# Kernel optimization log

Measured on AMD Instinct MI355X. Metric: run time of the kernel, lower is better.

The kernel has to match this reference:

```python
import jax, jax.numpy as jnp
import numpy as np

B, SQ, SK, D, H = 4, 2048, 2048, 1024, 16
HD = D // H
LN_EPS = 1e-5


def setup_inputs() -> dict:
    key = jax.random.key(0)
    ks = jax.random.split(key, 16)
    s = 0.02
    return {
        "query": jax.random.normal(ks[0], (B, SQ, D), jnp.float32),
        "key": jax.random.normal(ks[1], (B, SK, D), jnp.float32),
        "value": jax.random.normal(ks[2], (B, SK, D), jnp.float32),
        "attention_mask": jax.random.randint(ks[3], (B, 1, 1, SK), 0, 2, jnp.int32),
        "relative_position_bias": jax.random.normal(ks[4], (1, H, SQ, SK), jnp.float32) * s,
        "Wq": jax.random.normal(ks[5], (D, D), jnp.float32) * s,
        "bq": jnp.zeros((D,), jnp.float32),
        "Wk": jax.random.normal(ks[6], (D, D), jnp.float32) * s,
        "bk": jnp.zeros((D,), jnp.float32),
        "Wv": jax.random.normal(ks[7], (D, D), jnp.float32) * s,
        "bv": jnp.zeros((D,), jnp.float32),
        "Wo": jax.random.normal(ks[8], (D, D), jnp.float32) * s,
        "bo": jnp.zeros((D,), jnp.float32),
        "ln_gamma": jnp.ones((D,), jnp.float32),
        "ln_beta": jnp.zeros((D,), jnp.float32),
    }


def reference(query, key, value, attention_mask, relative_position_bias,
              Wq, bq, Wk, bk, Wv, bv, Wo, bo, ln_gamma, ln_beta):
    # projections (torch Linear: x @ W.T + b)
    q = query @ Wq.T + bq   # [B,Sq,D]
    k = key @ Wk.T + bk     # [B,Sk,D]
    v = value @ Wv.T + bv   # [B,Sk,D]
    # split heads -> [B,H,S,hd]
    q = q.reshape(B, SQ, H, HD).transpose(0, 2, 1, 3)
    k = k.reshape(B, SK, H, HD).transpose(0, 2, 1, 3)
    v = v.reshape(B, SK, H, HD).transpose(0, 2, 1, 3)
    scores = jnp.einsum('bhqd,bhkd->bhqk', q, k) / jnp.sqrt(jnp.float32(HD))
    scores = scores + relative_position_bias
    scores = jnp.where(attention_mask == 0, -jnp.inf, scores)
    weights = jax.nn.softmax(scores, axis=-1)  # [B,H,Sq,Sk]
    ctx = jnp.einsum('bhqk,bhkd->bhqd', weights, v)
    ctx = ctx.transpose(0, 2, 1, 3).reshape(B, SQ, D)
    out = ctx @ Wo.T + bo
    x = query + out
    mu = jnp.mean(x, axis=-1, keepdims=True)
    var = jnp.var(x, axis=-1, keepdims=True)
    return (x - mu) * jax.lax.rsqrt(var + LN_EPS) * ln_gamma + ln_beta
```

## Files before the change

kernel.cpp:

```cpp
#include <hip/hip_runtime.h>
#include <hip/hip_bf16.h>

#define B_   4
#define SQ_  2048
#define SK_  2048
#define D_   1024
#define H_   16
#define HD_  64

#define LOG2E 1.4426950408889634f

typedef __bf16 bf16_t;
typedef bf16_t bf16x8 __attribute__((ext_vector_type(8)));
typedef bf16_t bf16x4 __attribute__((ext_vector_type(4)));
typedef float  f32x4  __attribute__((ext_vector_type(4)));
typedef int    i32x4  __attribute__((ext_vector_type(4)));
typedef unsigned u32x2 __attribute__((ext_vector_type(2)));



__device__ __forceinline__ void gll16(const bf16_t* g, bf16_t* l) {
    __builtin_amdgcn_global_load_lds(
        (const __attribute__((address_space(1))) unsigned int*)g,
        (__attribute__((address_space(3))) unsigned int*)l, 16, 0, 0);
}
__device__ __forceinline__ void gll16f(const float* g, float* l) {
    __builtin_amdgcn_global_load_lds(
        (const __attribute__((address_space(1))) unsigned int*)g,
        (__attribute__((address_space(3))) unsigned int*)l, 16, 0, 0);
}

__global__ __launch_bounds__(256) void cvt_bf16(
    const float* __restrict__ p0, const float* __restrict__ p1,
    const float* __restrict__ p2, const float* __restrict__ p3,
    bf16_t* __restrict__ d, int n)
{
    int y = blockIdx.y;
    const float* s = (y == 0) ? p0 : (y == 1) ? p1 : (y == 2) ? p2 : p3;
    int i = (blockIdx.x * 256 + threadIdx.x) * 8;
    f32x4 a = *(const f32x4*)(s + i);
    f32x4 b = *(const f32x4*)(s + i + 4);
    bf16x8 o;
    #pragma unroll
    for (int j = 0; j < 4; j++) { o[j] = (bf16_t)a[j]; o[4 + j] = (bf16_t)b[j]; }
    *(bf16x8*)(d + (size_t)y * n + i) = o;
}

__global__ __launch_bounds__(256) void gemm_qkv(
    const float* __restrict__ xq, const float* __restrict__ xk, const float* __restrict__ xv,
    const bf16_t* __restrict__ wb,
    const float* __restrict__ bq, const float* __restrict__ bk, const float* __restrict__ bv,
    bf16_t* __restrict__ oq, bf16_t* __restrict__ ok, bf16_t* __restrict__ ov)
{
    __shared__ __align__(16) float  lAf[2][4096];
    __shared__ __align__(16) bf16_t lB[2][4096];

    int z = blockIdx.z;
    const float* A = (z == 0) ? xq : (z == 1) ? xk : xv;
    const bf16_t* Bm = wb + (size_t)z * 1024 * 1024;
    const float* bias = (z == 0) ? bq : (z == 1) ? bk : bv;
    bf16_t* out = (z == 0) ? oq : (z == 1) ? ok : ov;

    int tid = threadIdx.x;
    int w = tid >> 6, l = tid & 63, lr = l & 15, lg = l >> 4;
    int m0 = blockIdx.x * 128, n0 = blockIdx.y * 128;
    int wm = (w >> 1) * 64, wn = (w & 1) * 64;

    f32x4 zero4 = {0.f, 0.f, 0.f, 0.f};
    f32x4 acc[4][4];
    #pragma unroll
    for (int i = 0; i < 4; i++)
        #pragma unroll
        for (int j = 0; j < 4; j++) acc[i][j] = zero4;

    int as0 = tid, as1 = tid + 256, as2 = tid + 512, as3 = tid + 768;
    int ar0 = as0 >> 3, ar1 = as1 >> 3, ar2 = as2 >> 3, ar3 = as3 >> 3;
    const float* a_p0 = A + (size_t)(m0 + ar0) * 1024 + (((as0 & 7) ^ (ar0 & 7)) * 4);
    const float* a_p1 = A + (size_t)(m0 + ar1) * 1024 + (((as1 & 7) ^ (ar1 & 7)) * 4);
    const float* a_p2 = A + (size_t)(m0 + ar2) * 1024 + (((as2 & 7) ^ (ar2 & 7)) * 4);
    const float* a_p3 = A + (size_t)(m0 + ar3) * 1024 + (((as3 & 7) ^ (ar3 & 7)) * 4);

    int bs0 = tid, bs1 = tid + 256;
    int br0 = bs0 >> 2, br1 = bs1 >> 2;
    const bf16_t* b_p0 = Bm + (size_t)(n0 + br0) * 1024 + (((bs0 & 3) ^ ((br0 >> 1) & 3)) * 8);
    const bf16_t* b_p1 = Bm + (size_t)(n0 + br1) * 1024 + (((bs1 & 3) ^ ((br1 >> 1) & 3)) * 8);

    auto stage = [&](int buf, int kt) {
        gll16f(a_p0 + kt * 32, &lAf[buf][as0 * 4]);
        gll16f(a_p1 + kt * 32, &lAf[buf][as1 * 4]);
        gll16f(a_p2 + kt * 32, &lAf[buf][as2 * 4]);
        gll16f(a_p3 + kt * 32, &lAf[buf][as3 * 4]);
        gll16(b_p0 + kt * 32, &lB[buf][bs0 * 8]);
        gll16(b_p1 + kt * 32, &lB[buf][bs1 * 8]);
    };

    stage(0, 0);
    int buf = 0;
    #pragma unroll 1
    for (int kt = 0; kt < 32; ++kt) {
        __syncthreads();
        if (kt + 1 < 32) stage(buf ^ 1, kt + 1);
        bf16x8 af[4], bfr[4];
        #pragma unroll
        for (int i = 0; i < 4; i++) {
            int ra = wm + i * 16 + lr;
            int e = ra & 7;
            const float* arow = &lAf[buf][ra * 32];
            f32x4 lo = *(const f32x4*)(arow + ((( lg * 2)      ^ e) * 4));
            f32x4 hi = *(const f32x4*)(arow + ((((lg * 2) + 1) ^ e) * 4));
            bf16x8 a8;
            #pragma unroll
            for (int j = 0; j < 4; j++) { a8[j] = (bf16_t)lo[j]; a8[4 + j] = (bf16_t)hi[j]; }
            af[i] = a8;
            int rb = wn + i * 16 + lr;
            bfr[i] = *(const bf16x8*)&lB[buf][rb * 32 + ((lg ^ ((rb >> 1) & 3)) * 8)];
        }
        #pragma unroll
        for (int mi = 0; mi < 4; mi++)
            #pragma unroll
            for (int ni = 0; ni < 4; ni++)
                acc[mi][ni] = __builtin_amdgcn_mfma_f32_16x16x32_bf16(af[mi], bfr[ni], acc[mi][ni], 0, 0, 0);
        buf ^= 1;
    }

    #pragma unroll
    for (int mi = 0; mi < 4; mi++) {
        int row = m0 + wm + mi * 16 + lg * 4;
        int bb_ = row >> 11;
        int s   = row & 2047;
        #pragma unroll
        for (int ni = 0; ni < 4; ni++) {
            int col = n0 + wn + ni * 16 + lr;
            int hh = col >> 6, d6 = col & 63;
            float bval = bias[col];
            if (z == 0) {
                size_t obase = (((size_t)bb_ * H_ + hh) * SQ_ + s) * HD_ + d6;
                #pragma unroll
                for (int r = 0; r < 4; r++)
                    out[obase + (size_t)r * HD_] =
                        (bf16_t)((acc[mi][ni][r] + bval) * (0.125f * LOG2E));
            } else if (z == 1) {
                int kt = s >> 6, kpb = s & 63;
                size_t tb = (((size_t)bb_ * H_ + hh) * 32 + kt) * 4096;
                #pragma unroll
                for (int r = 0; r < 4; r++) {
                    int kp = kpb + r;
                    out[tb + (size_t)kp * 64 + (((d6 >> 3) ^ (kp & 7)) * 8) + (d6 & 7)] =
                        (bf16_t)(acc[mi][ni][r] + bval);
                }
            } else {
                int kt = s >> 6, kpb = s & 63;
                int chunk = ((kpb >> 5) & 1) * 4 + ((kpb >> 2) & 3);
                int jb    = ((kpb >> 4) & 1) * 4;
                size_t tb = (((size_t)bb_ * H_ + hh) * 32 + kt) * 4096;
                bf16x4 o4;
                #pragma unroll
                for (int r = 0; r < 4; r++) o4[r] = (bf16_t)(acc[mi][ni][r] + bval);
                *(bf16x4*)(out + tb + (size_t)d6 * 64 + ((chunk ^ (d6 & 7)) * 8) + jb) = o4;
            }
        }
    }
}

__global__ __launch_bounds__(256) void gemm_out(
    const bf16_t* __restrict__ A, const bf16_t* __restrict__ Bm,
    const float* __restrict__ bias, const float* __restrict__ resid,
    bf16_t* __restrict__ out)
{
    __shared__ __align__(16) bf16_t lA[2][4096];
    __shared__ __align__(16) bf16_t lB[2][4096];

    int tid = threadIdx.x;
    int w = tid >> 6, l = tid & 63, lr = l & 15, lg = l >> 4;
    int m0 = blockIdx.x * 128, n0 = blockIdx.y * 128;
    int wm = (w >> 1) * 64, wn = (w & 1) * 64;

    f32x4 zero4 = {0.f, 0.f, 0.f, 0.f};
    f32x4 acc[4][4];
    #pragma unroll
    for (int i = 0; i < 4; i++)
        #pragma unroll
        for (int j = 0; j < 4; j++) acc[i][j] = zero4;

    int s0 = tid, s1 = 256 + tid;
    int r0 = s0 >> 2, c0 = s0 & 3, r1 = s1 >> 2, c1 = s1 & 3;
    const bf16_t* a0 = A + (size_t)(m0 + r0) * 1024 + ((c0 ^ ((r0 >> 1) & 3)) * 8);
    const bf16_t* a1 = A + (size_t)(m0 + r1) * 1024 + ((c1 ^ ((r1 >> 1) & 3)) * 8);
    const bf16_t* b0 = Bm + (size_t)(n0 + r0) * 1024 + ((c0 ^ ((r0 >> 1) & 3)) * 8);
    const bf16_t* b1 = Bm + (size_t)(n0 + r1) * 1024 + ((c1 ^ ((r1 >> 1) & 3)) * 8);

    auto stage = [&](int buf, int kt) {
        gll16(a0 + kt * 32, &lA[buf][s0 * 8]);
        gll16(a1 + kt * 32, &lA[buf][s1 * 8]);
        gll16(b0 + kt * 32, &lB[buf][s0 * 8]);
        gll16(b1 + kt * 32, &lB[buf][s1 * 8]);
    };

    stage(0, 0);
    int buf = 0;
    #pragma unroll 1
    for (int kt = 0; kt < 32; ++kt) {
        __syncthreads();
        if (kt + 1 < 32) stage(buf ^ 1, kt + 1);
        bf16x8 af[4], bfr[4];
        #pragma unroll
        for (int i = 0; i < 4; i++) {
            int ra = wm + i * 16 + lr;
            af[i] = *(const bf16x8*)&lA[buf][ra * 32 + ((lg ^ ((ra >> 1) & 3)) * 8)];
            int rb = wn + i * 16 + lr;
            bfr[i] = *(const bf16x8*)&lB[buf][rb * 32 + ((lg ^ ((rb >> 1) & 3)) * 8)];
        }
        #pragma unroll
        for (int mi = 0; mi < 4; mi++)
            #pragma unroll
            for (int ni = 0; ni < 4; ni++)
                acc[mi][ni] = __builtin_amdgcn_mfma_f32_16x16x32_bf16(af[mi], bfr[ni], acc[mi][ni], 0, 0, 0);
        buf ^= 1;
    }

    #pragma unroll
    for (int mi = 0; mi < 4; mi++) {
        int row = m0 + wm + mi * 16 + lg * 4;
        #pragma unroll
        for (int ni = 0; ni < 4; ni++) {
            int col = n0 + wn + ni * 16 + lr;
            float bval = bias[col];
            #pragma unroll
            for (int r = 0; r < 4; r++) {
                size_t o = (size_t)(row + r) * D_ + col;
                out[o] = (bf16_t)(acc[mi][ni][r] + bval + resid[o]);
            }
        }
    }
}

__global__ __launch_bounds__(256) void attn_kernel(
    const bf16_t* __restrict__ qg, const bf16_t* __restrict__ kgt,
    const bf16_t* __restrict__ vgt, const float* __restrict__ bias,
    const int* __restrict__ mask, bf16_t* __restrict__ ctx)
{
    __shared__ __align__(16) bf16_t ksh[2][8192];
    __shared__ __align__(16) bf16_t vsh[2][8192];
    __shared__ __align__(8) unsigned char mlds[256];

    int x = blockIdx.x;
    int g8 = x & 7;
    int rest = x >> 3;
    int b  = rest & 3;
    int tt = ((rest >> 2) << 3) | g8;
    int h  = tt >> 4;
    int qt = tt & 15;

    int tid = threadIdx.x;
    int w   = tid >> 6;
    int l   = tid & 63;
    int q16 = l & 15;
    int g   = l >> 4;
    int g4  = g * 4;

    int qrow0 = qt * 128 + w * 16 + q16;
    int qrow1 = qrow0 + 64;
    const bf16_t* qbase = qg + ((size_t)b * H_ + h) * SQ_ * HD_;
    bf16x8 qf00 = *(const bf16x8*)(qbase + (size_t)qrow0 * HD_ + g * 8);
    bf16x8 qf01 = *(const bf16x8*)(qbase + (size_t)qrow0 * HD_ + 32 + g * 8);
    bf16x8 qf10 = *(const bf16x8*)(qbase + (size_t)qrow1 * HD_ + g * 8);
    bf16x8 qf11 = *(const bf16x8*)(qbase + (size_t)qrow1 * HD_ + 32 + g * 8);

    const bf16_t* kt_base = kgt + ((size_t)b * H_ + h) * 32 * 4096;
    const bf16_t* vt_base = vgt + ((size_t)b * H_ + h) * 32 * 4096;
    const float* bias_row0 = bias + ((size_t)h * SQ_ + qrow0) * SK_;
    const float* bias_row1 = bias + ((size_t)h * SQ_ + qrow1) * SK_;

    f32x4 zero4 = {0.f, 0.f, 0.f, 0.f};
    f32x4 oacc0[4], oacc1[4];
    #pragma unroll
    for (int i = 0; i < 4; i++) { oacc0[i] = zero4; oacc1[i] = zero4; }
    f32x4 lacc0 = zero4, lacc1 = zero4;

    bf16x8 ones;
    #pragma unroll
    for (int i = 0; i < 8; i++) ones[i] = (bf16_t)1.0f;

    auto stagePair = [&](int buf, int pt) {
        const bf16_t* ks = kt_base + (size_t)pt * 8192 + tid * 8;
        const bf16_t* vs = vt_base + (size_t)pt * 8192 + tid * 8;
        #pragma unroll
        for (int c = 0; c < 4; c++) {
            gll16(ks + c * 2048, &ksh[buf][c * 2048 + tid * 8]);
            gll16(vs + c * 2048, &vsh[buf][c * 2048 + tid * 8]);
        }
    };

    auto body = [&](const bf16_t* kb, const bf16_t* vb, int t) {
        f32x4 bb0[4], bb1[4];
        const float* bp0 = bias_row0 + t * 64 + g4;
        const float* bp1 = bias_row1 + t * 64 + g4;
        #pragma unroll
        for (int ni = 0; ni < 4; ni++) {
            bb0[ni] = *(const f32x4*)(bp0 + ni * 16);
            bb1[ni] = *(const f32x4*)(bp1 + ni * 16);
        }
        u32x2 mm = *(const u32x2*)&mlds[t * 8];
        unsigned lo = mm[0], hi = mm[1];

        f32x4 s0[4], s1[4];
        __builtin_amdgcn_s_setprio(1);
        #pragma unroll
        for (int ni = 0; ni < 4; ni++) {
            int krow = ni * 16 + q16;
            const bf16_t* kr = kb + krow * 64;
            bf16x8 kf0 = *(const bf16x8*)(kr + ((g       ^ (krow & 7)) * 8));
            bf16x8 kf1 = *(const bf16x8*)(kr + (((4 + g) ^ (krow & 7)) * 8));
            s0[ni] = zero4; s1[ni] = zero4;
            s0[ni] = __builtin_amdgcn_mfma_f32_16x16x32_bf16(kf0, qf00, s0[ni], 0, 0, 0);
            s0[ni] = __builtin_amdgcn_mfma_f32_16x16x32_bf16(kf1, qf01, s0[ni], 0, 0, 0);
            s1[ni] = __builtin_amdgcn_mfma_f32_16x16x32_bf16(kf0, qf10, s1[ni], 0, 0, 0);
            s1[ni] = __builtin_amdgcn_mfma_f32_16x16x32_bf16(kf1, qf11, s1[ni], 0, 0, 0);
        }
        __builtin_amdgcn_s_setprio(0);

        unsigned n0_ = (lo >> g4) & 0xF;
        unsigned n1_ = (lo >> (16 + g4)) & 0xF;
        unsigned n2_ = (hi >> g4) & 0xF;
        unsigned n3_ = (hi >> (16 + g4)) & 0xF;

        bf16x8 pA0, pA1, pB0, pB1;
        #pragma unroll
        for (int r = 0; r < 4; r++) {
            float b00 = ((n0_ >> r) & 1) ? bb0[0][r] : -30000.f;
            float b01 = ((n1_ >> r) & 1) ? bb0[1][r] : -30000.f;
            float b02 = ((n2_ >> r) & 1) ? bb0[2][r] : -30000.f;
            float b03 = ((n3_ >> r) & 1) ? bb0[3][r] : -30000.f;
            pA0[r]     = (bf16_t)__builtin_amdgcn_exp2f(fmaf(b00, LOG2E, s0[0][r]));
            pA0[4 + r] = (bf16_t)__builtin_amdgcn_exp2f(fmaf(b01, LOG2E, s0[1][r]));
            pA1[r]     = (bf16_t)__builtin_amdgcn_exp2f(fmaf(b02, LOG2E, s0[2][r]));
            pA1[4 + r] = (bf16_t)__builtin_amdgcn_exp2f(fmaf(b03, LOG2E, s0[3][r]));
            float b10 = ((n0_ >> r) & 1) ? bb1[0][r] : -30000.f;
            float b11 = ((n1_ >> r) & 1) ? bb1[1][r] : -30000.f;
            float b12 = ((n2_ >> r) & 1) ? bb1[2][r] : -30000.f;
            float b13 = ((n3_ >> r) & 1) ? bb1[3][r] : -30000.f;
            pB0[r]     = (bf16_t)__builtin_amdgcn_exp2f(fmaf(b10, LOG2E, s1[0][r]));
            pB0[4 + r] = (bf16_t)__builtin_amdgcn_exp2f(fmaf(b11, LOG2E, s1[1][r]));
            pB1[r]     = (bf16_t)__builtin_amdgcn_exp2f(fmaf(b12, LOG2E, s1[2][r]));
            pB1[4 + r] = (bf16_t)__builtin_amdgcn_exp2f(fmaf(b13, LOG2E, s1[3][r]));
        }

        __builtin_amdgcn_s_setprio(1);
        lacc0 = __builtin_amdgcn_mfma_f32_16x16x32_bf16(ones, pA0, lacc0, 0, 0, 0);
        lacc0 = __builtin_amdgcn_mfma_f32_16x16x32_bf16(ones, pA1, lacc0, 0, 0, 0);
        lacc1 = __builtin_amdgcn_mfma_f32_16x16x32_bf16(ones, pB0, lacc1, 0, 0, 0);
        lacc1 = __builtin_amdgcn_mfma_f32_16x16x32_bf16(ones, pB1, lacc1, 0, 0, 0);
        #pragma unroll
        for (int nd = 0; nd < 4; nd++) {
            int vrow = nd * 16 + q16;
            const bf16_t* vr = vb + vrow * 64;
            bf16x8 vf0 = *(const bf16x8*)(vr + ((g       ^ (vrow & 7)) * 8));
            bf16x8 vf1 = *(const bf16x8*)(vr + (((4 + g) ^ (vrow & 7)) * 8));
            oacc0[nd] = __builtin_amdgcn_mfma_f32_16x16x32_bf16(vf0, pA0, oacc0[nd], 0, 0, 0);
            oacc0[nd] = __builtin_amdgcn_mfma_f32_16x16x32_bf16(vf1, pA1, oacc0[nd], 0, 0, 0);
            oacc1[nd] = __builtin_amdgcn_mfma_f32_16x16x32_bf16(vf0, pB0, oacc1[nd], 0, 0, 0);
            oacc1[nd] = __builtin_amdgcn_mfma_f32_16x16x32_bf16(vf1, pB1, oacc1[nd], 0, 0, 0);
        }
        __builtin_amdgcn_s_setprio(0);
    };

    stagePair(0, 0);
    {
        const int* mp = mask + (size_t)b * SK_ + tid * 8;
        i32x4 u0 = *(const i32x4*)mp;
        i32x4 u1 = *(const i32x4*)(mp + 4);
        unsigned by = 0;
        #pragma unroll
        for (int j = 0; j < 4; j++) by |= (u0[j] != 0 ? 1u : 0u) << j;
        #pragma unroll
        for (int j = 0; j < 4; j++) by |= (u1[j] != 0 ? 1u : 0u) << (4 + j);
        mlds[tid] = (unsigned char)by;
    }
    __syncthreads();

    #pragma unroll 1
    for (int pt = 0; pt < 16; ++pt) {
        int buf = pt & 1;
        if (pt + 1 < 16) stagePair(buf ^ 1, pt + 1);
        body(&ksh[buf][0],    &vsh[buf][0],    2 * pt);
        body(&ksh[buf][4096], &vsh[buf][4096], 2 * pt + 1);
        __syncthreads();
    }

    float l_r0 = lacc0[0];
    float l_r1 = lacc1[0];
    float inv0 = (l_r0 > 0.f) ? 1.0f / l_r0 : 0.f;
    float inv1 = (l_r1 > 0.f) ? 1.0f / l_r1 : 0.f;

    bf16_t* cp0 = ctx + ((size_t)b * SQ_ + qrow0) * D_ + (size_t)h * HD_;
    bf16_t* cp1 = ctx + ((size_t)b * SQ_ + qrow1) * D_ + (size_t)h * HD_;
    #pragma unroll
    for (int nd = 0; nd < 4; nd++) {
        bf16x4 o4, o5;
        #pragma unroll
        for (int r = 0; r < 4; r++) {
            o4[r] = (bf16_t)(oacc0[nd][r] * inv0);
            o5[r] = (bf16_t)(oacc1[nd][r] * inv1);
        }
        *(bf16x4*)(cp0 + nd * 16 + g4) = o4;
        *(bf16x4*)(cp1 + nd * 16 + g4) = o5;
    }
}

__global__ __launch_bounds__(256) void ln_kernel(
    const bf16_t* __restrict__ x, const float* __restrict__ gamma,
    const float* __restrict__ beta, float* __restrict__ out)
{
    int row = blockIdx.x;
    int t = threadIdx.x;
    const bf16_t* src = x + (size_t)row * D_;
    bf16x4 v4 = *(const bf16x4*)(src + t * 4);
    f32x4 v;
    #pragma unroll
    for (int i = 0; i < 4; i++) v[i] = (float)v4[i];
    float s  = v[0] + v[1] + v[2] + v[3];
    float s2 = v[0] * v[0] + v[1] * v[1] + v[2] * v[2] + v[3] * v[3];
    #pragma unroll
    for (int off = 32; off > 0; off >>= 1) {
        s  += __shfl_down(s, off);
        s2 += __shfl_down(s2, off);
    }
    __shared__ float red[8];
    int w = t >> 6, l = t & 63;
    if (l == 0) { red[w] = s; red[4 + w] = s2; }
    __syncthreads();
    if (t == 0) {
        red[0] = red[0] + red[1] + red[2] + red[3];
        red[4] = red[4] + red[5] + red[6] + red[7];
    }
    __syncthreads();
    float mu  = red[0] * (1.0f / D_);
    float var = red[4] * (1.0f / D_) - mu * mu;
    float rstd = rsqrtf(var + 1e-5f);
    f32x4 g  = *(const f32x4*)(gamma + t * 4);
    f32x4 be = *(const f32x4*)(beta + t * 4);
    f32x4 o;
    #pragma unroll
    for (int i = 0; i < 4; i++) o[i] = (v[i] - mu) * rstd * g[i] + be[i];
    *(f32x4*)(out + (size_t)row * D_ + t * 4) = o;
}

extern "C" void kernel_launch(void* const* d_in, const int* in_sizes, int n_in,
                              void* d_out, int out_size, void* d_ws, size_t ws_size,
                              hipStream_t stream)
{
    const float* query = (const float*)d_in[0];
    const float* key   = (const float*)d_in[1];
    const float* value = (const float*)d_in[2];
    const int*   mask  = (const int*)d_in[3];
    const float* bias  = (const float*)d_in[4];
    const float* Wq    = (const float*)d_in[5];
    const float* bq    = (const float*)d_in[6];
    const float* Wk    = (const float*)d_in[7];
    const float* bk    = (const float*)d_in[8];
    const float* Wv    = (const float*)d_in[9];
    const float* bv    = (const float*)d_in[10];
    const float* Wo    = (const float*)d_in[11];
    const float* bo    = (const float*)d_in[12];
    const float* gamma = (const float*)d_in[13];
    const float* beta  = (const float*)d_in[14];
    float* out = (float*)d_out;

    char* ws = (char*)d_ws;
    const size_t MB = 1024 * 1024;
    bf16_t* ctx = (bf16_t*)(ws);
    bf16_t* tmp = (bf16_t*)(ws + 16 * MB);
    bf16_t* wb  = (bf16_t*)(ws + 48 * MB);
    bf16_t* qb  = (bf16_t*)(ws + 56 * MB);
    bf16_t* kgt = (bf16_t*)(ws + 72 * MB);
    bf16_t* vgt = (bf16_t*)(ws + 88 * MB);

    cvt_bf16<<<dim3(512, 4), 256, 0, stream>>>(Wq, Wk, Wv, Wo, wb, 1024 * 1024);
    gemm_qkv<<<dim3(64, 8, 3), 256, 0, stream>>>(query, key, value, wb,
                                                 bq, bk, bv, qb, kgt, vgt);
    attn_kernel<<<dim3(1024), 256, 0, stream>>>(qb, kgt, vgt, bias, mask, ctx);
    gemm_out<<<dim3(64, 8), 256, 0, stream>>>(ctx, wb + (size_t)3 * 1024 * 1024, bo, query, tmp);
    ln_kernel<<<dim3(8192), 256, 0, stream>>>(tmp, gamma, beta, out);
}
```

Measured before the change: 304.9 us.

## Use 8 waves per attention block with one 16-row query tile each

The attention kernel moves from 256 threads (4 waves, each handling two 16-row query tiles) to 512 threads (8 waves, each handling one tile). This halves per-wave accumulator and score registers and halves the per-thread share of K/V staging loads, trading register-level reuse of each K/V LDS fragment across two query tiles for more waves to hide latency. Mask packing is restricted to the first 256 threads to keep the same layout.

```diff
diff --git a/kernel.cpp b/kernel.cpp
--- a/kernel.cpp
+++ b/kernel.cpp
@@ -234,7 +234,7 @@
     }
 }
 
-__global__ __launch_bounds__(256) void attn_kernel(
+__global__ __launch_bounds__(512) void attn_kernel(
     const bf16_t* __restrict__ qg, const bf16_t* __restrict__ kgt,
     const bf16_t* __restrict__ vgt, const float* __restrict__ bias,
     const int* __restrict__ mask, bf16_t* __restrict__ ctx)
@@ -258,24 +258,20 @@
     int g   = l >> 4;
     int g4  = g * 4;
 
-    int qrow0 = qt * 128 + w * 16 + q16;
-    int qrow1 = qrow0 + 64;
+    int qrow = qt * 128 + w * 16 + q16;
     const bf16_t* qbase = qg + ((size_t)b * H_ + h) * SQ_ * HD_;
-    bf16x8 qf00 = *(const bf16x8*)(qbase + (size_t)qrow0 * HD_ + g * 8);
-    bf16x8 qf01 = *(const bf16x8*)(qbase + (size_t)qrow0 * HD_ + 32 + g * 8);
-    bf16x8 qf10 = *(const bf16x8*)(qbase + (size_t)qrow1 * HD_ + g * 8);
-    bf16x8 qf11 = *(const bf16x8*)(qbase + (size_t)qrow1 * HD_ + 32 + g * 8);
+    bf16x8 qf0 = *(const bf16x8*)(qbase + (size_t)qrow * HD_ + g * 8);
+    bf16x8 qf1 = *(const bf16x8*)(qbase + (size_t)qrow * HD_ + 32 + g * 8);
 
     const bf16_t* kt_base = kgt + ((size_t)b * H_ + h) * 32 * 4096;
     const bf16_t* vt_base = vgt + ((size_t)b * H_ + h) * 32 * 4096;
-    const float* bias_row0 = bias + ((size_t)h * SQ_ + qrow0) * SK_;
-    const float* bias_row1 = bias + ((size_t)h * SQ_ + qrow1) * SK_;
+    const float* bias_row = bias + ((size_t)h * SQ_ + qrow) * SK_;
 
     f32x4 zero4 = {0.f, 0.f, 0.f, 0.f};
-    f32x4 oacc0[4], oacc1[4];
-    #pragma unroll
-    for (int i = 0; i < 4; i++) { oacc0[i] = zero4; oacc1[i] = zero4; }
-    f32x4 lacc0 = zero4, lacc1 = zero4;
+    f32x4 oacc[4];
+    #pragma unroll
+    for (int i = 0; i < 4; i++) oacc[i] = zero4;
+    f32x4 lacc = zero4;
 
     bf16x8 ones;
     #pragma unroll
@@ -285,25 +281,21 @@
         const bf16_t* ks = kt_base + (size_t)pt * 8192 + tid * 8;
         const bf16_t* vs = vt_base + (size_t)pt * 8192 + tid * 8;
         #pragma unroll
-        for (int c = 0; c < 4; c++) {
-            gll16(ks + c * 2048, &ksh[buf][c * 2048 + tid * 8]);
-            gll16(vs + c * 2048, &vsh[buf][c * 2048 + tid * 8]);
+        for (int c = 0; c < 2; c++) {
+            gll16(ks + c * 4096, &ksh[buf][c * 4096 + tid * 8]);
+            gll16(vs + c * 4096, &vsh[buf][c * 4096 + tid * 8]);
         }
     };
 
     auto body = [&](const bf16_t* kb, const bf16_t* vb, int t) {
-        f32x4 bb0[4], bb1[4];
-        const float* bp0 = bias_row0 + t * 64 + g4;
-        const float* bp1 = bias_row1 + t * 64 + g4;
-        #pragma unroll
-        for (int ni = 0; ni < 4; ni++) {
-            bb0[ni] = *(const f32x4*)(bp0 + ni * 16);
-            bb1[ni] = *(const f32x4*)(bp1 + ni * 16);
-        }
+        f32x4 bb[4];
+        const float* bp = bias_row + t * 64 + g4;
+        #pragma unroll
+        for (int ni = 0; ni < 4; ni++) bb[ni] = *(const f32x4*)(bp + ni * 16);
         u32x2 mm = *(const u32x2*)&mlds[t * 8];
         unsigned lo = mm[0], hi = mm[1];
 
-        f32x4 s0[4], s1[4];
+        f32x4 s0[4];
         __builtin_amdgcn_s_setprio(1);
         #pragma unroll
         for (int ni = 0; ni < 4; ni++) {
@@ -311,11 +303,9 @@
             const bf16_t* kr = kb + krow * 64;
             bf16x8 kf0 = *(const bf16x8*)(kr + ((g       ^ (krow & 7)) * 8));
             bf16x8 kf1 = *(const bf16x8*)(kr + (((4 + g) ^ (krow & 7)) * 8));
-            s0[ni] = zero4; s1[ni] = zero4;
-            s0[ni] = __builtin_amdgcn_mfma_f32_16x16x32_bf16(kf0, qf00, s0[ni], 0, 0, 0);
-            s0[ni] = __builtin_amdgcn_mfma_f32_16x16x32_bf16(kf1, qf01, s0[ni], 0, 0, 0);
-            s1[ni] = __builtin_amdgcn_mfma_f32_16x16x32_bf16(kf0, qf10, s1[ni], 0, 0, 0);
-            s1[ni] = __builtin_amdgcn_mfma_f32_16x16x32_bf16(kf1, qf11, s1[ni], 0, 0, 0);
+            s0[ni] = zero4;
+            s0[ni] = __builtin_amdgcn_mfma_f32_16x16x32_bf16(kf0, qf0, s0[ni], 0, 0, 0);
+            s0[ni] = __builtin_amdgcn_mfma_f32_16x16x32_bf16(kf1, qf1, s0[ni], 0, 0, 0);
         }
         __builtin_amdgcn_s_setprio(0);
 
@@ -324,48 +314,36 @@
         unsigned n2_ = (hi >> g4) & 0xF;
         unsigned n3_ = (hi >> (16 + g4)) & 0xF;
 
-        bf16x8 pA0, pA1, pB0, pB1;
+        bf16x8 pA0, pA1;
         #pragma unroll
         for (int r = 0; r < 4; r++) {
-            float b00 = ((n0_ >> r) & 1) ? bb0[0][r] : -30000.f;
-            float b01 = ((n1_ >> r) & 1) ? bb0[1][r] : -30000.f;
-            float b02 = ((n2_ >> r) & 1) ? bb0[2][r] : -30000.f;
-            float b03 = ((n3_ >> r) & 1) ? bb0[3][r] : -30000.f;
-            pA0[r]     = (bf16_t)__builtin_amdgcn_exp2f(fmaf(b00, LOG2E, s0[0][r]));
-            pA0[4 + r] = (bf16_t)__builtin_amdgcn_exp2f(fmaf(b01, LOG2E, s0[1][r]));
-            pA1[r]     = (bf16_t)__builtin_amdgcn_exp2f(fmaf(b02, LOG2E, s0[2][r]));
-            pA1[4 + r] = (bf16_t)__builtin_amdgcn_exp2f(fmaf(b03, LOG2E, s0[3][r]));
-            float b10 = ((n0_ >> r) & 1) ? bb1[0][r] : -30000.f;
-            float b11 = ((n1_ >> r) & 1) ? bb1[1][r] : -30000.f;
-            float b12 = ((n2_ >> r) & 1) ? bb1[2][r] : -30000.f;
-            float b13 = ((n3_ >> r) & 1) ? bb1[3][r] : -30000.f;
-            pB0[r]     = (bf16_t)__builtin_amdgcn_exp2f(fmaf(b10, LOG2E, s1[0][r]));
-            pB0[4 + r] = (bf16_t)__builtin_amdgcn_exp2f(fmaf(b11, LOG2E, s1[1][r]));
-            pB1[r]     = (bf16_t)__builtin_amdgcn_exp2f(fmaf(b12, LOG2E, s1[2][r]));
-            pB1[4 + r] = (bf16_t)__builtin_amdgcn_exp2f(fmaf(b13, LOG2E, s1[3][r]));
+            float b0 = ((n0_ >> r) & 1) ? bb[0][r] : -30000.f;
+            float b1 = ((n1_ >> r) & 1) ? bb[1][r] : -30000.f;
+            float b2 = ((n2_ >> r) & 1) ? bb[2][r] : -30000.f;
+            float b3 = ((n3_ >> r) & 1) ? bb[3][r] : -30000.f;
+            pA0[r]     = (bf16_t)__builtin_amdgcn_exp2f(fmaf(b0, LOG2E, s0[0][r]));
+            pA0[4 + r] = (bf16_t)__builtin_amdgcn_exp2f(fmaf(b1, LOG2E, s0[1][r]));
+            pA1[r]     = (bf16_t)__builtin_amdgcn_exp2f(fmaf(b2, LOG2E, s0[2][r]));
+            pA1[4 + r] = (bf16_t)__builtin_amdgcn_exp2f(fmaf(b3, LOG2E, s0[3][r]));
         }
 
         __builtin_amdgcn_s_setprio(1);
-        lacc0 = __builtin_amdgcn_mfma_f32_16x16x32_bf16(ones, pA0, lacc0, 0, 0, 0);
-        lacc0 = __builtin_amdgcn_mfma_f32_16x16x32_bf16(ones, pA1, lacc0, 0, 0, 0);
-        lacc1 = __builtin_amdgcn_mfma_f32_16x16x32_bf16(ones, pB0, lacc1, 0, 0, 0);
-        lacc1 = __builtin_amdgcn_mfma_f32_16x16x32_bf16(ones, pB1, lacc1, 0, 0, 0);
+        lacc = __builtin_amdgcn_mfma_f32_16x16x32_bf16(ones, pA0, lacc, 0, 0, 0);
+        lacc = __builtin_amdgcn_mfma_f32_16x16x32_bf16(ones, pA1, lacc, 0, 0, 0);
         #pragma unroll
         for (int nd = 0; nd < 4; nd++) {
             int vrow = nd * 16 + q16;
             const bf16_t* vr = vb + vrow * 64;
             bf16x8 vf0 = *(const bf16x8*)(vr + ((g       ^ (vrow & 7)) * 8));
             bf16x8 vf1 = *(const bf16x8*)(vr + (((4 + g) ^ (vrow & 7)) * 8));
-            oacc0[nd] = __builtin_amdgcn_mfma_f32_16x16x32_bf16(vf0, pA0, oacc0[nd], 0, 0, 0);
-            oacc0[nd] = __builtin_amdgcn_mfma_f32_16x16x32_bf16(vf1, pA1, oacc0[nd], 0, 0, 0);
-            oacc1[nd] = __builtin_amdgcn_mfma_f32_16x16x32_bf16(vf0, pB0, oacc1[nd], 0, 0, 0);
-            oacc1[nd] = __builtin_amdgcn_mfma_f32_16x16x32_bf16(vf1, pB1, oacc1[nd], 0, 0, 0);
+            oacc[nd] = __builtin_amdgcn_mfma_f32_16x16x32_bf16(vf0, pA0, oacc[nd], 0, 0, 0);
+            oacc[nd] = __builtin_amdgcn_mfma_f32_16x16x32_bf16(vf1, pA1, oacc[nd], 0, 0, 0);
         }
         __builtin_amdgcn_s_setprio(0);
     };
 
     stagePair(0, 0);
-    {
+    if (tid < 256) {
         const int* mp = mask + (size_t)b * SK_ + tid * 8;
         i32x4 u0 = *(const i32x4*)mp;
         i32x4 u1 = *(const i32x4*)(mp + 4);
@@ -387,23 +365,16 @@
         __syncthreads();
     }
 
-    float l_r0 = lacc0[0];
-    float l_r1 = lacc1[0];
-    float inv0 = (l_r0 > 0.f) ? 1.0f / l_r0 : 0.f;
-    float inv1 = (l_r1 > 0.f) ? 1.0f / l_r1 : 0.f;
-
-    bf16_t* cp0 = ctx + ((size_t)b * SQ_ + qrow0) * D_ + (size_t)h * HD_;
-    bf16_t* cp1 = ctx + ((size_t)b * SQ_ + qrow1) * D_ + (size_t)h * HD_;
+    float l_r = lacc[0];
+    float inv = (l_r > 0.f) ? 1.0f / l_r : 0.f;
+
+    bf16_t* cp = ctx + ((size_t)b * SQ_ + qrow) * D_ + (size_t)h * HD_;
     #pragma unroll
     for (int nd = 0; nd < 4; nd++) {
-        bf16x4 o4, o5;
-        #pragma unroll
-        for (int r = 0; r < 4; r++) {
-            o4[r] = (bf16_t)(oacc0[nd][r] * inv0);
-            o5[r] = (bf16_t)(oacc1[nd][r] * inv1);
-        }
-        *(bf16x4*)(cp0 + nd * 16 + g4) = o4;
-        *(bf16x4*)(cp1 + nd * 16 + g4) = o5;
+        bf16x4 o4;
+        #pragma unroll
+        for (int r = 0; r < 4; r++) o4[r] = (bf16_t)(oacc[nd][r] * inv);
+        *(bf16x4*)(cp + nd * 16 + g4) = o4;
     }
 }
 
@@ -478,7 +449,7 @@
     cvt_bf16<<<dim3(512, 4), 256, 0, stream>>>(Wq, Wk, Wv, Wo, wb, 1024 * 1024);
     gemm_qkv<<<dim3(64, 8, 3), 256, 0, stream>>>(query, key, value, wb,
                                                  bq, bk, bv, qb, kgt, vgt);
-    attn_kernel<<<dim3(1024), 256, 0, stream>>>(qb, kgt, vgt, bias, mask, ctx);
+    attn_kernel<<<dim3(1024), 512, 0, stream>>>(qb, kgt, vgt, bias, mask, ctx);
     gemm_out<<<dim3(64, 8), 256, 0, stream>>>(ctx, wb + (size_t)3 * 1024 * 1024, bo, query, tmp);
     ln_kernel<<<dim3(8192), 256, 0, stream>>>(tmp, gamma, beta, out);
 }
```

After: 303.8 us, median of 3. No clear change (-0.4%).
